# Optimization experiments

Measured on AMD Instinct MI355X. Metric: run time of the kernel, lower is better.

Reference implementation:

```python
import jax, jax.numpy as jnp
import numpy as np

NEG = -1000000.0  # mask fill value used by the torch module

def setup_inputs() -> dict:
    key = jax.random.key(0)
    ks = jax.random.split(key, 7)
    B, Tq, Tk, Din, H, Dv = 16, 128, 256, 64, 256, 256
    return {
        "queries": jax.random.normal(ks[0], (B, Tq, Din), dtype=jnp.float32),
        "keys": jax.random.normal(ks[1], (B, Tk, Din), dtype=jnp.float32),
        "values": jax.random.normal(ks[2], (B, Tk, Dv), dtype=jnp.float32),
        "valid_lens": jax.random.randint(ks[3], (B,), 0, Tk, dtype=jnp.int32),
        "wq": jax.random.normal(ks[4], (Din, H), dtype=jnp.float32) * 0.05,
        "wk": jax.random.normal(ks[5], (Din, H), dtype=jnp.float32) * 0.05,
        "wv": jax.random.normal(ks[6], (H,), dtype=jnp.float32) * 0.05,
    }

def reference(queries, keys, values, valid_lens, wq, wk, wv):
    # Project queries and keys to num_hiddens
    q = jnp.einsum("bqd,dh->bqh", queries, wq)       # [B,Tq,H]
    k = jnp.einsum("bkd,dh->bkh", keys, wk)          # [B,Tk,H]
    # Additive features [B,Tq,Tk,H] -> tanh -> scalar score via wv
    feats = jnp.tanh(q[:, :, None, :] + k[:, None, :, :])
    scores = jnp.einsum("bqkh,h->bqk", feats, wv)    # [B,Tq,Tk]
    # Masked softmax over last axis; valid_lens [B] broadcasts over Tq
    Tk = scores.shape[-1]
    mask = jnp.arange(Tk)[None, None, :] < valid_lens[:, None, None]
    scores = jnp.where(mask, scores, NEG)
    attn = jax.nn.softmax(scores, axis=-1)           # [B,Tq,Tk]
    return jnp.einsum("bqk,bkv->bqv", attn, values)  # [B,Tq,Dv]
```

## Files before the change

### kernel.cpp

```cpp
#include <hip/hip_runtime.h>

#define B_  16
#define TQ  128
#define TK  256
#define DIN 64
#define H_  256
#define DV  256
#define HT  8
#define QT  4
#define NW  8
#define NEG -1000000.0f

#define SCALE  2.8853900817779268f
#define LOG2E  1.4426950408889634f

typedef float v2f __attribute__((ext_vector_type(2)));

__device__ inline float fast_exp2(float x) { return __builtin_amdgcn_exp2f(x); }
__device__ inline float fast_rcp(float x)  { return __builtin_amdgcn_rcpf(x); }
__device__ inline v2f v2fma(v2f a, v2f b, v2f c) {
    return __builtin_elementwise_fma(a, b, c);
}

__global__ __launch_bounds__(256) void proj_kernel(
    const float* __restrict__ keys, const float* __restrict__ wk,
    const float* __restrict__ queries, const float* __restrict__ wq,
    float* __restrict__ EkT, float4* __restrict__ EqW,
    const int* __restrict__ valid_lens)
{
    int bx = blockIdx.x;
    int t  = threadIdx.x;
    if (bx < 512) {
        int b  = bx >> 5;
        int h0 = (bx & 31) * HT;
        int vlC = (valid_lens[b] + 63) & ~63;
        if (t >= vlC) return;
        const float4* krow4 = (const float4*)(keys + (size_t)(b * TK + t) * DIN);
        float acc[HT];
        #pragma unroll
        for (int hh = 0; hh < HT; ++hh) acc[hh] = 0.f;
        #pragma unroll 4
        for (int d4 = 0; d4 < DIN / 4; ++d4) {
            float4 kd = krow4[d4];
            const float* wrow = wk + 4 * d4 * H_ + h0;
            #pragma unroll
            for (int hh = 0; hh < HT; ++hh) acc[hh] = fmaf(kd.x, wrow[hh], acc[hh]);
            #pragma unroll
            for (int hh = 0; hh < HT; ++hh) acc[hh] = fmaf(kd.y, wrow[H_ + hh], acc[hh]);
            #pragma unroll
            for (int hh = 0; hh < HT; ++hh) acc[hh] = fmaf(kd.z, wrow[2 * H_ + hh], acc[hh]);
            #pragma unroll
            for (int hh = 0; hh < HT; ++hh) acc[hh] = fmaf(kd.w, wrow[3 * H_ + hh], acc[hh]);
        }
        #pragma unroll
        for (int hh = 0; hh < HT; ++hh)
            EkT[(b * H_ + h0 + hh) * TK + t] = fast_exp2(acc[hh] * SCALE);
    } else {
        int i = bx - 512;
        int b = i >> 5;
        int g = i & 31;
        const float* qbase = queries + (size_t)(b * TQ + 4 * g) * DIN;
        float a0 = 0.f, a1 = 0.f, a2 = 0.f, a3 = 0.f;
        #pragma unroll
        for (int d = 0; d < DIN; ++d) {
            float ww = wq[d * H_ + t];
            a0 = fmaf(qbase[d],           ww, a0);
            a1 = fmaf(qbase[DIN + d],     ww, a1);
            a2 = fmaf(qbase[2 * DIN + d], ww, a2);
            a3 = fmaf(qbase[3 * DIN + d], ww, a3);
        }
        EqW[(size_t)(b * 32 + g) * H_ + t] =
            make_float4(fast_exp2(a0 * SCALE), fast_exp2(a1 * SCALE),
                        fast_exp2(a2 * SCALE), fast_exp2(a3 * SCALE));
    }
}

__device__ inline float waveMax(float v) {
    #pragma unroll
    for (int off = 32; off > 0; off >>= 1) v = fmaxf(v, __shfl_xor(v, off, 64));
    return v;
}
__device__ inline float waveSum(float v) {
    #pragma unroll
    for (int off = 32; off > 0; off >>= 1) v += __shfl_xor(v, off, 64);
    return v;
}

__global__ __launch_bounds__(512, 4) void attn_kernel(
    const float4* __restrict__ EqW, const float* __restrict__ EkT,
    const float* __restrict__ values, const int* __restrict__ valid_lens,
    const float* __restrict__ wv, float* __restrict__ out)
{
    __shared__ float scoreP[NW][QT][TK];
    __shared__ float attnT[TK][QT];

    int bx  = blockIdx.x;
    int xcd = bx & 7;
    int i   = bx >> 3;
    int b   = xcd + 8 * (i & 1);
    int g   = i >> 1;
    int q0  = g * QT;
    int t   = threadIdx.x;
    int w   = t >> 6, l = t & 63;
    int vl  = valid_lens[b];

    {
        const float4* eqb = EqW + (size_t)(b * 32 + g) * H_;
        const float4* ek4 = (const float4*)(EkT + (size_t)b * H_ * TK);
        int h0 = __builtin_amdgcn_readfirstlane(w) * (H_ / NW);
        v2f sA0={0,0}, sA1={0,0}, sB0={0,0}, sB1={0,0};
        v2f sC0={0,0}, sC1={0,0}, sD0={0,0}, sD1={0,0};
        const v2f one2 = {1.f, 1.f};

        auto row = [&](float eq, v2f kxy, v2f kzw, v2f w2, v2f& sp0, v2f& sp1) {
            v2f e2 = {eq, eq};
            v2f d0 = v2fma(e2, kxy, one2);
            v2f d1 = v2fma(e2, kzw, one2);
            float rp0 = fast_rcp(d0.x * d0.y);
            float rp1 = fast_rcp(d1.x * d1.y);
            v2f r0 = (v2f){d0.y, d0.x} * (v2f){rp0, rp0};
            v2f r1 = (v2f){d1.y, d1.x} * (v2f){rp1, rp1};
            sp0 = v2fma(w2, r0, sp0);
            sp1 = v2fma(w2, r1, sp1);
        };

        auto body = [&](int h, float4 kv) {
            float4 eq  = eqb[h];
            float  wvh = wv[h];
            v2f w2  = {wvh, wvh};
            v2f kxy = {kv.x, kv.y};
            v2f kzw = {kv.z, kv.w};
            row(eq.x, kxy, kzw, w2, sA0, sA1);
            row(eq.y, kxy, kzw, w2, sB0, sB1);
            row(eq.z, kxy, kzw, w2, sC0, sC1);
            row(eq.w, kxy, kzw, w2, sD0, sD1);
        };

        float4 kv0 = ek4[(size_t)h0 * (TK / 4) + l];
        float4 kv1 = ek4[(size_t)(h0 + 1) * (TK / 4) + l];
        #pragma unroll 2
        for (int hh = 0; hh < H_ / NW - 2; ++hh) {
            float4 kvn = ek4[(size_t)(h0 + hh + 2) * (TK / 4) + l];
            body(h0 + hh, kv0);
            kv0 = kv1; kv1 = kvn;
        }
        body(h0 + H_ / NW - 2, kv0);
        body(h0 + H_ / NW - 1, kv1);

        ((float4*)&scoreP[w][0][0])[l] = make_float4(sA0.x, sA0.y, sA1.x, sA1.y);
        ((float4*)&scoreP[w][1][0])[l] = make_float4(sB0.x, sB0.y, sB1.x, sB1.y);
        ((float4*)&scoreP[w][2][0])[l] = make_float4(sC0.x, sC0.y, sC1.x, sC1.y);
        ((float4*)&scoreP[w][3][0])[l] = make_float4(sD0.x, sD0.y, sD1.x, sD1.y);
    }
    __syncthreads();

    if (t < 64 * QT) {
        int r = w;
        float W = waveSum(wv[l] + wv[l + 64] + wv[l + 128] + wv[l + 192]);
        float4 v = {0, 0, 0, 0};
        #pragma unroll
        for (int s = 0; s < NW; ++s) {
            float4 ps = ((const float4*)&scoreP[s][r][0])[l];
            v.x += ps.x; v.y += ps.y; v.z += ps.z; v.w += ps.w;
        }
        int k0 = 4 * l;
        v.x = (k0     < vl) ? fmaf(-2.f, v.x, W) : NEG;
        v.y = (k0 + 1 < vl) ? fmaf(-2.f, v.y, W) : NEG;
        v.z = (k0 + 2 < vl) ? fmaf(-2.f, v.z, W) : NEG;
        v.w = (k0 + 3 < vl) ? fmaf(-2.f, v.w, W) : NEG;
        float m  = waveMax(fmaxf(fmaxf(v.x, v.y), fmaxf(v.z, v.w)));
        float p0 = fast_exp2((v.x - m) * LOG2E);
        float p1 = fast_exp2((v.y - m) * LOG2E);
        float p2 = fast_exp2((v.z - m) * LOG2E);
        float p3 = fast_exp2((v.w - m) * LOG2E);
        float dr = fast_rcp(waveSum(p0 + p1 + p2 + p3));
        attnT[k0    ][r] = p0 * dr;
        attnT[k0 + 1][r] = p1 * dr;
        attnT[k0 + 2][r] = p2 * dr;
        attnT[k0 + 3][r] = p3 * dr;
    }
    __syncthreads();

    {
        int half = t >> 8, v = t & 255;
        int kLim = (vl == 0) ? TK : vl;
        int kBeg = half * (TK / 2);
        int kEnd = min(kBeg + TK / 2, kLim);
        const float*  vcol = values + (size_t)b * TK * DV + v;
        const float4* at4  = (const float4*)attnT;
        float o0 = 0.f, o1 = 0.f, o2 = 0.f, o3 = 0.f;
        #pragma unroll 4
        for (int k = kBeg; k < kEnd; ++k) {
            float  vv = vcol[k * DV];
            float4 a  = at4[k];
            o0 = fmaf(a.x, vv, o0);
            o1 = fmaf(a.y, vv, o1);
            o2 = fmaf(a.z, vv, o2);
            o3 = fmaf(a.w, vv, o3);
        }
        if (half == 1) {
            scoreP[0][0][v] = o0;
            scoreP[0][1][v] = o1;
            scoreP[0][2][v] = o2;
            scoreP[0][3][v] = o3;
        }
        __syncthreads();
        if (half == 0) {
            float* orow = out + (size_t)(b * TQ + q0) * DV + v;
            orow[0]      = o0 + scoreP[0][0][v];
            orow[DV]     = o1 + scoreP[0][1][v];
            orow[2 * DV] = o2 + scoreP[0][2][v];
            orow[3 * DV] = o3 + scoreP[0][3][v];
        }
    }
}

extern "C" void kernel_launch(void* const* d_in, const int* in_sizes, int n_in,
                              void* d_out, int out_size, void* d_ws, size_t ws_size,
                              hipStream_t stream) {
    const float* queries    = (const float*)d_in[0];
    const float* keys       = (const float*)d_in[1];
    const float* values     = (const float*)d_in[2];
    const int*   valid_lens = (const int*)  d_in[3];
    const float* wq         = (const float*)d_in[4];
    const float* wk         = (const float*)d_in[5];
    const float* wv         = (const float*)d_in[6];
    float* out = (float*)d_out;

    float*  EkT = (float*)d_ws;
    float4* EqW = (float4*)(EkT + (size_t)B_ * H_ * TK);

    proj_kernel<<<1024, 256, 0, stream>>>(keys, wk, queries, wq, EkT, EqW, valid_lens);
    attn_kernel<<<B_ * (TQ / QT), 512, 0, stream>>>(EqW, EkT, values,
                                                    valid_lens, wv, out);
}
```

Baseline: 96.61 us.

## Use persistent attention blocks with atomic work queue and skip masked key halves

The attention kernel becomes persistent: 512 blocks pull (batch, query-pair) items from an atomic counter that the projection kernel resets. Query tile size drops from 4 to 2. The score loop now skips work on key columns beyond valid_len, handling only the first half of keys when valid_len is at most 128 and skipping scoring entirely when it is zero. The aim is to balance work across CUs despite varying valid lengths and to avoid useless tanh work. The cost is atomic and extra barrier overhead per item, and less EqW/EkT reuse per item.

```diff
diff --git a/kernel.cpp b/kernel.cpp
--- a/kernel.cpp
+++ b/kernel.cpp
@@ -7,8 +7,9 @@
 #define H_  256
 #define DV  256
 #define HT  8
-#define QT  4
+#define QT  2
 #define NW  8
+#define NITEMS (B_ * TQ / QT)
 #define NEG -1000000.0f
 
 #define SCALE  2.8853900817779268f
@@ -26,7 +27,7 @@
     const float* __restrict__ keys, const float* __restrict__ wk,
     const float* __restrict__ queries, const float* __restrict__ wq,
     float* __restrict__ EkT, float4* __restrict__ EqW,
-    const int* __restrict__ valid_lens)
+    const int* __restrict__ valid_lens, int* __restrict__ qcounter)
 {
     int bx = blockIdx.x;
     int t  = threadIdx.x;
@@ -56,6 +57,7 @@
         for (int hh = 0; hh < HT; ++hh)
             EkT[(b * H_ + h0 + hh) * TK + t] = fast_exp2(acc[hh] * SCALE);
     } else {
+        if (bx == 512 && t == 0) *qcounter = 0;
         int i = bx - 512;
         int b = i >> 5;
         int g = i & 31;
@@ -86,132 +88,149 @@
     return v;
 }
 
-__global__ __launch_bounds__(512, 4) void attn_kernel(
+__global__ __launch_bounds__(512, 2) void attn_kernel(
     const float4* __restrict__ EqW, const float* __restrict__ EkT,
     const float* __restrict__ values, const int* __restrict__ valid_lens,
-    const float* __restrict__ wv, float* __restrict__ out)
+    const float* __restrict__ wv, float* __restrict__ out,
+    int* __restrict__ qcounter)
 {
-    __shared__ float scoreP[NW][QT][TK];
-    __shared__ float attnT[TK][QT];
-
-    int bx  = blockIdx.x;
-    int xcd = bx & 7;
-    int i   = bx >> 3;
-    int b   = xcd + 8 * (i & 1);
-    int g   = i >> 1;
-    int q0  = g * QT;
-    int t   = threadIdx.x;
-    int w   = t >> 6, l = t & 63;
-    int vl  = valid_lens[b];
-
-    {
-        const float4* eqb = EqW + (size_t)(b * 32 + g) * H_;
-        const float4* ek4 = (const float4*)(EkT + (size_t)b * H_ * TK);
-        int h0 = __builtin_amdgcn_readfirstlane(w) * (H_ / NW);
-        v2f sA0={0,0}, sA1={0,0}, sB0={0,0}, sB1={0,0};
-        v2f sC0={0,0}, sC1={0,0}, sD0={0,0}, sD1={0,0};
-        const v2f one2 = {1.f, 1.f};
-
-        auto row = [&](float eq, v2f kxy, v2f kzw, v2f w2, v2f& sp0, v2f& sp1) {
-            v2f e2 = {eq, eq};
-            v2f d0 = v2fma(e2, kxy, one2);
-            v2f d1 = v2fma(e2, kzw, one2);
-            float rp0 = fast_rcp(d0.x * d0.y);
-            float rp1 = fast_rcp(d1.x * d1.y);
-            v2f r0 = (v2f){d0.y, d0.x} * (v2f){rp0, rp0};
-            v2f r1 = (v2f){d1.y, d1.x} * (v2f){rp1, rp1};
-            sp0 = v2fma(w2, r0, sp0);
-            sp1 = v2fma(w2, r1, sp1);
-        };
-
-        auto body = [&](int h, float4 kv) {
-            float4 eq  = eqb[h];
-            float  wvh = wv[h];
-            v2f w2  = {wvh, wvh};
-            v2f kxy = {kv.x, kv.y};
-            v2f kzw = {kv.z, kv.w};
-            row(eq.x, kxy, kzw, w2, sA0, sA1);
-            row(eq.y, kxy, kzw, w2, sB0, sB1);
-            row(eq.z, kxy, kzw, w2, sC0, sC1);
-            row(eq.w, kxy, kzw, w2, sD0, sD1);
-        };
-
-        float4 kv0 = ek4[(size_t)h0 * (TK / 4) + l];
-        float4 kv1 = ek4[(size_t)(h0 + 1) * (TK / 4) + l];
-        #pragma unroll 2
-        for (int hh = 0; hh < H_ / NW - 2; ++hh) {
-            float4 kvn = ek4[(size_t)(h0 + hh + 2) * (TK / 4) + l];
-            body(h0 + hh, kv0);
-            kv0 = kv1; kv1 = kvn;
-        }
-        body(h0 + H_ / NW - 2, kv0);
-        body(h0 + H_ / NW - 1, kv1);
-
-        ((float4*)&scoreP[w][0][0])[l] = make_float4(sA0.x, sA0.y, sA1.x, sA1.y);
-        ((float4*)&scoreP[w][1][0])[l] = make_float4(sB0.x, sB0.y, sB1.x, sB1.y);
-        ((float4*)&scoreP[w][2][0])[l] = make_float4(sC0.x, sC0.y, sC1.x, sC1.y);
-        ((float4*)&scoreP[w][3][0])[l] = make_float4(sD0.x, sD0.y, sD1.x, sD1.y);
-    }
-    __syncthreads();
-
-    if (t < 64 * QT) {
-        int r = w;
-        float W = waveSum(wv[l] + wv[l + 64] + wv[l + 128] + wv[l + 192]);
-        float4 v = {0, 0, 0, 0};
-        #pragma unroll
-        for (int s = 0; s < NW; ++s) {
-            float4 ps = ((const float4*)&scoreP[s][r][0])[l];
-            v.x += ps.x; v.y += ps.y; v.z += ps.z; v.w += ps.w;
-        }
-        int k0 = 4 * l;
-        v.x = (k0     < vl) ? fmaf(-2.f, v.x, W) : NEG;
-        v.y = (k0 + 1 < vl) ? fmaf(-2.f, v.y, W) : NEG;
-        v.z = (k0 + 2 < vl) ? fmaf(-2.f, v.z, W) : NEG;
-        v.w = (k0 + 3 < vl) ? fmaf(-2.f, v.w, W) : NEG;
-        float m  = waveMax(fmaxf(fmaxf(v.x, v.y), fmaxf(v.z, v.w)));
-        float p0 = fast_exp2((v.x - m) * LOG2E);
-        float p1 = fast_exp2((v.y - m) * LOG2E);
-        float p2 = fast_exp2((v.z - m) * LOG2E);
-        float p3 = fast_exp2((v.w - m) * LOG2E);
-        float dr = fast_rcp(waveSum(p0 + p1 + p2 + p3));
-        attnT[k0    ][r] = p0 * dr;
-        attnT[k0 + 1][r] = p1 * dr;
-        attnT[k0 + 2][r] = p2 * dr;
-        attnT[k0 + 3][r] = p3 * dr;
-    }
-    __syncthreads();
-
-    {
-        int half = t >> 8, v = t & 255;
-        int kLim = (vl == 0) ? TK : vl;
-        int kBeg = half * (TK / 2);
-        int kEnd = min(kBeg + TK / 2, kLim);
-        const float*  vcol = values + (size_t)b * TK * DV + v;
-        const float4* at4  = (const float4*)attnT;
-        float o0 = 0.f, o1 = 0.f, o2 = 0.f, o3 = 0.f;
-        #pragma unroll 4
-        for (int k = kBeg; k < kEnd; ++k) {
-            float  vv = vcol[k * DV];
-            float4 a  = at4[k];
-            o0 = fmaf(a.x, vv, o0);
-            o1 = fmaf(a.y, vv, o1);
-            o2 = fmaf(a.z, vv, o2);
-            o3 = fmaf(a.w, vv, o3);
-        }
-        if (half == 1) {
-            scoreP[0][0][v] = o0;
-            scoreP[0][1][v] = o1;
-            scoreP[0][2][v] = o2;
-            scoreP[0][3][v] = o3;
-        }
-        __syncthreads();
-        if (half == 0) {
-            float* orow = out + (size_t)(b * TQ + q0) * DV + v;
-            orow[0]      = o0 + scoreP[0][0][v];
-            orow[DV]     = o1 + scoreP[0][1][v];
-            orow[2 * DV] = o2 + scoreP[0][2][v];
-            orow[3 * DV] = o3 + scoreP[0][3][v];
-        }
+    __shared__ float  scoreP[NW][QT][TK];
+    __shared__ float2 attnT2[TK];
+    __shared__ int    itemS;
+
+    int t = threadIdx.x;
+    int w = t >> 6, l = t & 63;
+    const v2f one2 = {1.f, 1.f};
+
+    for (;;) {
+        if (t == 0) itemS = atomicAdd(qcounter, 1);
+        __syncthreads();
+        int it = itemS;
+        if (it >= NITEMS) break;
+        int b  = it & (B_ - 1);
+        int g  = it >> 4;
+        int q0 = 2 * g;
+        int vl = valid_lens[b];
+
+        {
+            const float2* eqb = (const float2*)EqW
+                              + (size_t)(b * 32 + (g >> 1)) * H_ * 2 + (g & 1);
+            int h0 = __builtin_amdgcn_readfirstlane(w) * (H_ / NW);
+            int f2 = (vl == 0) ? 0 : ((vl > TK / 2) ? 2 : 1);
+
+            auto pair = [&](float eq, v2f k2, v2f w2, v2f& sp) {
+                v2f e2 = {eq, eq};
+                v2f d  = v2fma(e2, k2, one2);
+                float rp = fast_rcp(d.x * d.y);
+                v2f r  = (v2f){d.y, d.x} * (v2f){rp, rp};
+                sp = v2fma(w2, r, sp);
+            };
+
+            if (f2 == 2) {
+                const float2* ek2 = (const float2*)(EkT + (size_t)b * H_ * TK);
+                v2f s00 = {0,0}, s01 = {0,0}, s10 = {0,0}, s11 = {0,0};
+                auto body = [&](int h, float2 ka, float2 kb) {
+                    float2 eq  = eqb[2 * h];
+                    float  wvh = wv[h];
+                    v2f w2 = {wvh, wvh};
+                    v2f kA = {ka.x, ka.y}, kB = {kb.x, kb.y};
+                    pair(eq.x, kA, w2, s00);
+                    pair(eq.y, kA, w2, s10);
+                    pair(eq.x, kB, w2, s01);
+                    pair(eq.y, kB, w2, s11);
+                };
+                float2 ka0 = ek2[(size_t)h0 * (TK / 2) + l];
+                float2 kb0 = ek2[(size_t)h0 * (TK / 2) + 64 + l];
+                #pragma unroll 2
+                for (int hh = 0; hh < H_ / NW - 1; ++hh) {
+                    float2 ka1 = ek2[(size_t)(h0 + hh + 1) * (TK / 2) + l];
+                    float2 kb1 = ek2[(size_t)(h0 + hh + 1) * (TK / 2) + 64 + l];
+                    body(h0 + hh, ka0, kb0);
+                    ka0 = ka1; kb0 = kb1;
+                }
+                body(h0 + H_ / NW - 1, ka0, kb0);
+                ((float2*)&scoreP[w][0][0])[l]      = make_float2(s00.x, s00.y);
+                ((float2*)&scoreP[w][0][0])[l + 64] = make_float2(s01.x, s01.y);
+                ((float2*)&scoreP[w][1][0])[l]      = make_float2(s10.x, s10.y);
+                ((float2*)&scoreP[w][1][0])[l + 64] = make_float2(s11.x, s11.y);
+            } else if (f2 == 1) {
+                const float2* ek2 = (const float2*)(EkT + (size_t)b * H_ * TK);
+                v2f s00 = {0,0}, s10 = {0,0};
+                auto body = [&](int h, float2 ka) {
+                    float2 eq  = eqb[2 * h];
+                    float  wvh = wv[h];
+                    v2f w2 = {wvh, wvh};
+                    v2f kA = {ka.x, ka.y};
+                    pair(eq.x, kA, w2, s00);
+                    pair(eq.y, kA, w2, s10);
+                };
+                float2 ka0 = ek2[(size_t)h0 * (TK / 2) + l];
+                #pragma unroll 2
+                for (int hh = 0; hh < H_ / NW - 1; ++hh) {
+                    float2 ka1 = ek2[(size_t)(h0 + hh + 1) * (TK / 2) + l];
+                    body(h0 + hh, ka0);
+                    ka0 = ka1;
+                }
+                body(h0 + H_ / NW - 1, ka0);
+                ((float2*)&scoreP[w][0][0])[l] = make_float2(s00.x, s00.y);
+                ((float2*)&scoreP[w][1][0])[l] = make_float2(s10.x, s10.y);
+            }
+        }
+        __syncthreads();
+
+        if (t < 64 * QT) {
+            int r = w;
+            float W = waveSum(wv[l] + wv[l + 64] + wv[l + 128] + wv[l + 192]);
+            float4 v = {0, 0, 0, 0};
+            #pragma unroll
+            for (int s = 0; s < NW; ++s) {
+                float4 ps = ((const float4*)&scoreP[s][r][0])[l];
+                v.x += ps.x; v.y += ps.y; v.z += ps.z; v.w += ps.w;
+            }
+            int k0 = 4 * l;
+            v.x = (k0     < vl) ? fmaf(-2.f, v.x, W) : NEG;
+            v.y = (k0 + 1 < vl) ? fmaf(-2.f, v.y, W) : NEG;
+            v.z = (k0 + 2 < vl) ? fmaf(-2.f, v.z, W) : NEG;
+            v.w = (k0 + 3 < vl) ? fmaf(-2.f, v.w, W) : NEG;
+            float m  = waveMax(fmaxf(fmaxf(v.x, v.y), fmaxf(v.z, v.w)));
+            float p0 = fast_exp2((v.x - m) * LOG2E);
+            float p1 = fast_exp2((v.y - m) * LOG2E);
+            float p2 = fast_exp2((v.z - m) * LOG2E);
+            float p3 = fast_exp2((v.w - m) * LOG2E);
+            float dr = fast_rcp(waveSum(p0 + p1 + p2 + p3));
+            ((float*)&attnT2[k0    ])[r] = p0 * dr;
+            ((float*)&attnT2[k0 + 1])[r] = p1 * dr;
+            ((float*)&attnT2[k0 + 2])[r] = p2 * dr;
+            ((float*)&attnT2[k0 + 3])[r] = p3 * dr;
+        }
+        __syncthreads();
+
+        {
+            int half = t >> 8, v = t & 255;
+            int kLim = (vl == 0) ? TK : vl;
+            int kBeg = half * (TK / 2);
+            int kEnd = min(kBeg + TK / 2, kLim);
+            const float* vcol = values + (size_t)b * TK * DV + v;
+            float o0 = 0.f, o1 = 0.f;
+            #pragma unroll 4
+            for (int k = kBeg; k < kEnd; ++k) {
+                float  vv = vcol[k * DV];
+                float2 a  = attnT2[k];
+                o0 = fmaf(a.x, vv, o0);
+                o1 = fmaf(a.y, vv, o1);
+            }
+            if (half == 1) {
+                scoreP[0][0][v] = o0;
+                scoreP[0][1][v] = o1;
+            }
+            __syncthreads();
+            if (half == 0) {
+                float* orow = out + (size_t)(b * TQ + q0) * DV + v;
+                orow[0]  = o0 + scoreP[0][0][v];
+                orow[DV] = o1 + scoreP[0][1][v];
+            }
+        }
+        __syncthreads();
     }
 }
 
@@ -229,8 +248,10 @@
 
     float*  EkT = (float*)d_ws;
     float4* EqW = (float4*)(EkT + (size_t)B_ * H_ * TK);
-
-    proj_kernel<<<1024, 256, 0, stream>>>(keys, wk, queries, wq, EkT, EqW, valid_lens);
-    attn_kernel<<<B_ * (TQ / QT), 512, 0, stream>>>(EqW, EkT, values,
-                                                    valid_lens, wv, out);
-}
+    int* qcounter = (int*)(EqW + (size_t)B_ * 32 * H_);
+
+    proj_kernel<<<1024, 256, 0, stream>>>(keys, wk, queries, wq, EkT, EqW,
+                                          valid_lens, qcounter);
+    attn_kernel<<<512, 512, 0, stream>>>(EqW, EkT, values, valid_lens, wv, out,
+                                         qcounter);
+}
```

After: 121.4 us. +25.6%, slower.
